# Kernel tuning notes

Hardware: AMD Instinct MI355X
Metric: run time of the kernel (lower is better)

Reference implementation:

```python
import jax, jax.numpy as jnp
import numpy as np

NUM_USERS = 100000
NUM_ITEMS = 50000
EMBED_DIM = 64
N_LAYERS = 3
SOCIAL_LAYERS = 2
NNZ_R = 3200000
NNZ_S = 2000000


def setup_inputs() -> dict:
    key = jax.random.key(0)
    ks = jax.random.split(key, 8)
    return {
        "user_emb": jax.random.normal(ks[0], (NUM_USERS, EMBED_DIM), jnp.float32) * 0.1,
        "item_emb": jax.random.normal(ks[1], (NUM_ITEMS, EMBED_DIM), jnp.float32) * 0.1,
        "r_vals": jax.random.uniform(ks[2], (NNZ_R,), jnp.float32) * 0.01,
        "s_vals": jax.random.uniform(ks[3], (NNZ_S,), jnp.float32) * 0.01,
        "r_rows": jax.random.randint(ks[4], (NNZ_R,), 0, NUM_USERS),
        "r_cols": jax.random.randint(ks[5], (NNZ_R,), 0, NUM_ITEMS),
        "s_rows": jax.random.randint(ks[6], (NNZ_S,), 0, NUM_USERS),
        "s_cols": jax.random.randint(ks[7], (NNZ_S,), 0, NUM_USERS),
    }


def spmm(rows, cols, vals, x, n_rows):
    # sparse(COO) @ dense: out[r] += v * x[c]
    return jax.ops.segment_sum(vals[:, None] * x[cols], rows, num_segments=n_rows)


def l2_normalize(x, eps=1e-12):
    return x / jnp.maximum(jnp.linalg.norm(x, axis=1, keepdims=True), eps)


def reference(user_emb, item_emb, r_vals, s_vals, r_rows, r_cols, s_rows, s_cols):
    # LightGCN-style propagation over user-item bipartite graph
    u, i = user_emb, item_emb
    u_sum, i_sum = user_emb, item_emb
    for _ in range(N_LAYERS):
        u_next = spmm(r_rows, r_cols, r_vals, i, NUM_USERS)   # R @ item
        i_next = spmm(r_cols, r_rows, r_vals, u, NUM_ITEMS)   # R^T @ user
        u, i = u_next, i_next  # dropout = identity in eval mode
        u_sum = u_sum + u
        i_sum = i_sum + i
    user_final = u_sum / (N_LAYERS + 1)
    item_final = i_sum / (N_LAYERS + 1)

    # social graph propagation on user embeddings
    s = user_emb
    s_sum = user_emb
    for _ in range(SOCIAL_LAYERS):
        s = spmm(s_rows, s_cols, s_vals, s, NUM_USERS)
        s_sum = s_sum + s
    social_final = s_sum / (SOCIAL_LAYERS + 1)

    final_user = l2_normalize(0.6 * user_final + 0.4 * social_final)
    final_item = l2_normalize(item_final)
    return final_user, final_item
```

## Files before the change

### kernel.cpp

```cpp
#include <hip/hip_runtime.h>

constexpr int NUM_USERS = 100000;
constexpr int NUM_ITEMS = 50000;
constexpr int DIM = 64;
constexpr int NNZ_R = 3200000;
constexpr int NNZ_S = 2000000;
constexpr int NNZ_TOT = NNZ_R + NNZ_R + NNZ_S;

constexpr int BSH_U = 8, BROWS_U = 256;
constexpr int BSH_I = 7, BROWS_I = 128;
constexpr int NC_U = (NUM_USERS + BROWS_U - 1) / BROWS_U;
constexpr int NC_I = (NUM_ITEMS + BROWS_I - 1) / BROWS_I;
constexpr int NC_S = NC_U;
constexpr int NC = NC_U + NC_I + NC_S;
constexpr int NBLK = 256;
constexpr int NPB = NBLK * NC;
constexpr int CHUNK_R = NNZ_R / NBLK;
constexpr int CHUNK_S = (NNZ_S + NBLK - 1) / NBLK;

constexpr int SB_EDGES = 4096;
constexpr int SB_PAIRS = 8192;

__device__ __forceinline__ float bf2f(unsigned short u) {
    return __uint_as_float((unsigned)u << 16);
}
__device__ __forceinline__ unsigned short f2bf(float f) {
    unsigned u = __float_as_uint(f);
    return (unsigned short)((u + 0x7FFFu + ((u >> 16) & 1u)) >> 16);
}
__device__ __forceinline__ float bflo(unsigned r) { return __uint_as_float(r << 16); }
__device__ __forceinline__ float bfhi(unsigned r) { return __uint_as_float(r & 0xFFFF0000u); }

__global__ __launch_bounds__(1024) void hist_lds(const int* __restrict__ rr,
                                                 const int* __restrict__ rc,
                                                 const int* __restrict__ sr,
                                                 int* __restrict__ cntPB ) {
    __shared__ int lds[NC];
    int k = blockIdx.x, tid = threadIdx.x;
    for (int c = tid; c < NC; c += 1024) lds[c] = 0;
    __syncthreads();
    int r0 = k * CHUNK_R, r1 = r0 + CHUNK_R;
    int s0 = k * CHUNK_S, s1 = min(s0 + CHUNK_S, NNZ_S);
    for (int i = r0 + tid; i < r1; i += 1024) {
        atomicAdd(&lds[rr[i] >> BSH_U], 1);
        atomicAdd(&lds[NC_U + (rc[i] >> BSH_I)], 1);
    }
    for (int i = s0 + tid; i < s1; i += 1024)
        atomicAdd(&lds[NC_U + NC_I + (sr[i] >> BSH_U)], 1);
    __syncthreads();
    for (int c = tid; c < NC; c += 1024) cntPB[c * NBLK + k] = lds[c];
}

__global__ __launch_bounds__(NBLK) void scan_bkt(int* __restrict__ cntPB,
                                                 int* __restrict__ bktTot) {
    int c = blockIdx.x, t = threadIdx.x;
    __shared__ int sh[NBLK];
    int v = cntPB[c * NBLK + t];
    sh[t] = v;
    __syncthreads();
    for (int off = 1; off < NBLK; off <<= 1) {
        int u = (t >= off) ? sh[t - off] : 0;
        __syncthreads();
        sh[t] += u;
        __syncthreads();
    }
    cntPB[c * NBLK + t] = sh[t] - v;
    if (t == NBLK - 1) bktTot[c] = sh[t];
}

__global__ __launch_bounds__(1024) void scan_top(int* __restrict__ B ) {
    __shared__ int part[1024];
    int t = threadIdx.x;
    const int chunk = (NC + 1023) >> 10;
    int lo = t * chunk, hi = min(lo + chunk, NC);
    int s = 0;
    for (int i = lo; i < hi; ++i) s += B[i];
    part[t] = s;
    __syncthreads();
    for (int off = 1; off < 1024; off <<= 1) {
        int v = (t >= off) ? part[t - off] : 0;
        __syncthreads();
        part[t] += v;
        __syncthreads();
    }
    int excl = (t == 0) ? 0 : part[t - 1];
    for (int i = lo; i < hi; ++i) {
        int v = B[i];
        B[i] = excl;
        excl += v;
    }
    if (t == 1023) B[NC] = part[1023];
}

__global__ __launch_bounds__(1024) void bin_pass(const int* __restrict__ rr,
                                                 const int* __restrict__ rc,
                                                 const float* __restrict__ rv,
                                                 const int* __restrict__ sr,
                                                 const int* __restrict__ sc,
                                                 const float* __restrict__ sv,
                                                 const int* __restrict__ cntPB,
                                                 const int* __restrict__ bktBase,
                                                 int2* __restrict__ ent) {
    __shared__ int cur[NC];
    __shared__ int cnt[NC];
    __shared__ int lstart[NC];
    __shared__ int lcur[NC];
    __shared__ int part[1024];
    __shared__ int2 stage[SB_PAIRS];
    __shared__ int gaddr[SB_PAIRS];
    int k = blockIdx.x, tid = threadIdx.x;
    for (int c = tid; c < NC; c += 1024)
        cur[c] = bktBase[c] + cntPB[c * NBLK + k];

    int r0 = k * CHUNK_R;
    for (int sb = 0; sb < CHUNK_R; sb += SB_EDGES) {
        int nE = min(SB_EDGES, CHUNK_R - sb);
        int base = r0 + sb;
        for (int c = tid; c < NC; c += 1024) { cnt[c] = 0; lcur[c] = 0; }
        __syncthreads();
        for (int i = tid; i < nE; i += 1024) {
            atomicAdd(&cnt[rr[base + i] >> BSH_U], 1);
            atomicAdd(&cnt[NC_U + (rc[base + i] >> BSH_I)], 1);
        }
        __syncthreads();
        int o0 = 2 * tid, o1 = 2 * tid + 1;
        int a = (o0 < NC) ? cnt[o0] : 0;
        int b = (o1 < NC) ? cnt[o1] : 0;
        part[tid] = a + b;
        __syncthreads();
        for (int off = 1; off < 1024; off <<= 1) {
            int v = (tid >= off) ? part[tid - off] : 0;
            __syncthreads();
            part[tid] += v;
            __syncthreads();
        }
        int ex = (tid == 0) ? 0 : part[tid - 1];
        if (o0 < NC) lstart[o0] = ex;
        if (o1 < NC) lstart[o1] = ex + a;
        __syncthreads();
        for (int i = tid; i < nE; i += 1024) {
            int r = rr[base + i], c = rc[base + i];
            int v = __float_as_int(rv[base + i]);
            int cu_ = r >> BSH_U;
            int j = atomicAdd(&lcur[cu_], 1);
            int lp = lstart[cu_] + j;
            stage[lp] = make_int2(((r & (BROWS_U - 1)) << 17) | c, v);
            gaddr[lp] = cur[cu_] + j;
            int ci_ = NC_U + (c >> BSH_I);
            int j2 = atomicAdd(&lcur[ci_], 1);
            int lp2 = lstart[ci_] + j2;
            stage[lp2] = make_int2(((c & (BROWS_I - 1)) << 17) | r, v);
            gaddr[lp2] = cur[ci_] + j2;
        }
        __syncthreads();
        int nP = 2 * nE;
        for (int s = tid; s < nP; s += 1024)
            ent[gaddr[s]] = stage[s];
        for (int c = tid; c < NC; c += 1024) cur[c] += cnt[c];
        __syncthreads();
    }

    int s0 = k * CHUNK_S, sEnd = min(s0 + CHUNK_S, NNZ_S);
    for (int sb = s0; sb < sEnd; sb += SB_PAIRS) {
        int nE = min(SB_PAIRS, sEnd - sb);
        for (int c = tid; c < NC; c += 1024) { cnt[c] = 0; lcur[c] = 0; }
        __syncthreads();
        for (int i = tid; i < nE; i += 1024)
            atomicAdd(&cnt[NC_U + NC_I + (sr[sb + i] >> BSH_U)], 1);
        __syncthreads();
        int o0 = 2 * tid, o1 = 2 * tid + 1;
        int a = (o0 < NC) ? cnt[o0] : 0;
        int b = (o1 < NC) ? cnt[o1] : 0;
        part[tid] = a + b;
        __syncthreads();
        for (int off = 1; off < 1024; off <<= 1) {
            int v = (tid >= off) ? part[tid - off] : 0;
            __syncthreads();
            part[tid] += v;
            __syncthreads();
        }
        int ex = (tid == 0) ? 0 : part[tid - 1];
        if (o0 < NC) lstart[o0] = ex;
        if (o1 < NC) lstart[o1] = ex + a;
        __syncthreads();
        for (int i = tid; i < nE; i += 1024) {
            int r = sr[sb + i];
            int cs_ = NC_U + NC_I + (r >> BSH_U);
            int j = atomicAdd(&lcur[cs_], 1);
            int lp = lstart[cs_] + j;
            stage[lp] = make_int2(((r & (BROWS_U - 1)) << 17) | sc[sb + i],
                                  __float_as_int(sv[sb + i]));
            gaddr[lp] = cur[cs_] + j;
        }
        __syncthreads();
        for (int s = tid; s < nE; s += 1024)
            ent[gaddr[s]] = stage[s];
        for (int c = tid; c < NC; c += 1024) cur[c] += cnt[c];
        __syncthreads();
    }
}

__global__ __launch_bounds__(512) void sort_buckets(const int2* __restrict__ src,
                                                    int2* __restrict__ dst,
                                                    const int* __restrict__ bktBase,
                                                    int* __restrict__ rPu,
                                                    int* __restrict__ rPi,
                                                    int* __restrict__ rPs) {
    int gb = blockIdx.x;
    int* rowptr;
    int brows, lb, nrows;
    if (gb < NC_U)              { rowptr = rPu; brows = BROWS_U; lb = gb;               nrows = NUM_USERS; }
    else if (gb < NC_U + NC_I)  { rowptr = rPi; brows = BROWS_I; lb = gb - NC_U;        nrows = NUM_ITEMS; }
    else                        { rowptr = rPs; brows = BROWS_U; lb = gb - NC_U - NC_I; nrows = NUM_USERS; }
    int t = threadIdx.x;
    __shared__ int cnt[256];
    __shared__ int part[256];
    __shared__ int ofs[256];
    if (t < 256) cnt[t] = 0;
    __syncthreads();
    int b0 = bktBase[gb], b1 = bktBase[gb + 1];
    for (int i = b0 + t; i < b1; i += 512)
        atomicAdd(&cnt[(unsigned)src[i].x >> 17], 1);
    __syncthreads();
    if (t < 256) part[t] = cnt[t];
    __syncthreads();
    for (int off = 1; off < 256; off <<= 1) {
        int v = 0;
        if (t < 256 && t >= off) v = part[t - off];
        __syncthreads();
        if (t < 256) part[t] += v;
        __syncthreads();
    }
    if (t < 256) ofs[t] = part[t] - cnt[t];
    __syncthreads();
    int gr = lb * brows + t;
    if (t < brows && gr < nrows) rowptr[gr] = b0 + ofs[t];
    if (gb == 0 && t == 0) {
        rPu[NUM_USERS] = NNZ_R;
        rPi[NUM_ITEMS] = 2 * NNZ_R;
        rPs[NUM_USERS] = NNZ_TOT;
    }
    __syncthreads();
    for (int i = b0 + t; i < b1; i += 512) {
        int2 v = src[i];
        int lr = (unsigned)v.x >> 17;
        int pos = b0 + atomicAdd(&ofs[lr], 1);
        dst[pos] = make_int2(v.x & 0x1FFFF, v.y);
    }
}

struct SpmmOp {
    const int* rowptr;
    const int2* ent;
    const unsigned short* x;
    unsigned short* out;
    float* acc;
    float w;
    int nrows;
};

__global__ __launch_bounds__(256, 4) void spmm2(SpmmOp A, SpmmOp B, int ablocks) {
    bool isA = (int)blockIdx.x < ablocks;
    SpmmOp op = isA ? A : B;
    int bid = isA ? blockIdx.x : blockIdx.x - ablocks;
    int row = bid * 4 + (threadIdx.x >> 6);
    if (row >= op.nrows) return;
    int lane = threadIdx.x & 63;
    int g = lane >> 4;
    int q = lane & 15;
    const int2* __restrict__ ent = op.ent;
    const unsigned short* __restrict__ x = op.x;
    int e = op.rowptr[row], end = op.rowptr[row + 1];
    float s0 = 0.f, s1 = 0.f, s2 = 0.f, s3 = 0.f;
    for (; e + 16 <= end; e += 16) {
        int2 n0 = ent[e + g];
        int2 n1 = ent[e + 4 + g];
        int2 n2 = ent[e + 8 + g];
        int2 n3 = ent[e + 12 + g];
        uint2 r0 = *reinterpret_cast<const uint2*>(x + (size_t)n0.x * DIM + q * 4);
        uint2 r1 = *reinterpret_cast<const uint2*>(x + (size_t)n1.x * DIM + q * 4);
        uint2 r2 = *reinterpret_cast<const uint2*>(x + (size_t)n2.x * DIM + q * 4);
        uint2 r3 = *reinterpret_cast<const uint2*>(x + (size_t)n3.x * DIM + q * 4);
        float v0 = __int_as_float(n0.y), v1 = __int_as_float(n1.y);
        float v2 = __int_as_float(n2.y), v3 = __int_as_float(n3.y);
        s0 += v0 * bflo(r0.x); s1 += v0 * bfhi(r0.x); s2 += v0 * bflo(r0.y); s3 += v0 * bfhi(r0.y);
        s0 += v1 * bflo(r1.x); s1 += v1 * bfhi(r1.x); s2 += v1 * bflo(r1.y); s3 += v1 * bfhi(r1.y);
        s0 += v2 * bflo(r2.x); s1 += v2 * bfhi(r2.x); s2 += v2 * bflo(r2.y); s3 += v2 * bfhi(r2.y);
        s0 += v3 * bflo(r3.x); s1 += v3 * bfhi(r3.x); s2 += v3 * bflo(r3.y); s3 += v3 * bfhi(r3.y);
    }
    if (e < end) {
        int t0 = e + 4 * g;
        int lim = end - 1;
        int c0 = min(t0, lim),     c1 = min(t0 + 1, lim);
        int c2 = min(t0 + 2, lim), c3 = min(t0 + 3, lim);
        int2 n0 = ent[c0];
        int2 n1 = ent[c1];
        int2 n2 = ent[c2];
        int2 n3 = ent[c3];
        uint2 r0 = *reinterpret_cast<const uint2*>(x + (size_t)n0.x * DIM + q * 4);
        uint2 r1 = *reinterpret_cast<const uint2*>(x + (size_t)n1.x * DIM + q * 4);
        uint2 r2 = *reinterpret_cast<const uint2*>(x + (size_t)n2.x * DIM + q * 4);
        uint2 r3 = *reinterpret_cast<const uint2*>(x + (size_t)n3.x * DIM + q * 4);
        float v0 = (t0     < end) ? __int_as_float(n0.y) : 0.f;
        float v1 = (t0 + 1 < end) ? __int_as_float(n1.y) : 0.f;
        float v2 = (t0 + 2 < end) ? __int_as_float(n2.y) : 0.f;
        float v3 = (t0 + 3 < end) ? __int_as_float(n3.y) : 0.f;
        s0 += v0 * bflo(r0.x); s1 += v0 * bfhi(r0.x); s2 += v0 * bflo(r0.y); s3 += v0 * bfhi(r0.y);
        s0 += v1 * bflo(r1.x); s1 += v1 * bfhi(r1.x); s2 += v1 * bflo(r1.y); s3 += v1 * bfhi(r1.y);
        s0 += v2 * bflo(r2.x); s1 += v2 * bfhi(r2.x); s2 += v2 * bflo(r2.y); s3 += v2 * bfhi(r2.y);
        s0 += v3 * bflo(r3.x); s1 += v3 * bfhi(r3.x); s2 += v3 * bflo(r3.y); s3 += v3 * bfhi(r3.y);
    }
    s0 += __shfl_xor(s0, 16, 64); s0 += __shfl_xor(s0, 32, 64);
    s1 += __shfl_xor(s1, 16, 64); s1 += __shfl_xor(s1, 32, 64);
    s2 += __shfl_xor(s2, 16, 64); s2 += __shfl_xor(s2, 32, 64);
    s3 += __shfl_xor(s3, 16, 64); s3 += __shfl_xor(s3, 32, 64);
    if (g == 0) {
        size_t base = (size_t)row * DIM + q * 4;
        if (op.out) {
            uint2 o;
            o.x = (unsigned)f2bf(s0) | ((unsigned)f2bf(s1) << 16);
            o.y = (unsigned)f2bf(s2) | ((unsigned)f2bf(s3) << 16);
            *reinterpret_cast<uint2*>(op.out + base) = o;
        }
        float4* a = reinterpret_cast<float4*>(op.acc + base);
        float4 av = *a;
        av.x += op.w * s0; av.y += op.w * s1; av.z += op.w * s2; av.w += op.w * s3;
        *a = av;
    }
}

__global__ void init_acc(const float* __restrict__ ue, const float* __restrict__ ie,
                         float* __restrict__ accU, float* __restrict__ accI,
                         unsigned short* __restrict__ ueB, unsigned short* __restrict__ ieB,
                         int u4, int i4) {
    const float wu = 0.6f / 4.0f + 0.4f / 3.0f;
    const float wi = 0.25f;
    int i = blockIdx.x * blockDim.x + threadIdx.x;
    int st = gridDim.x * blockDim.x;
    int n4 = u4 + i4;
    for (; i < n4; i += st) {
        if (i < u4) {
            float4 v = reinterpret_cast<const float4*>(ue)[i];
            reinterpret_cast<float4*>(accU)[i] = make_float4(wu * v.x, wu * v.y, wu * v.z, wu * v.w);
            ushort4 b;
            b.x = f2bf(v.x); b.y = f2bf(v.y); b.z = f2bf(v.z); b.w = f2bf(v.w);
            reinterpret_cast<ushort4*>(ueB)[i] = b;
        } else {
            int j = i - u4;
            float4 v = reinterpret_cast<const float4*>(ie)[j];
            reinterpret_cast<float4*>(accI)[j] = make_float4(wi * v.x, wi * v.y, wi * v.z, wi * v.w);
            ushort4 b;
            b.x = f2bf(v.x); b.y = f2bf(v.y); b.z = f2bf(v.z); b.w = f2bf(v.w);
            reinterpret_cast<ushort4*>(ieB)[j] = b;
        }
    }
}

__global__ void finalize_kernel(float* __restrict__ out, int nrows) {
    int row = blockIdx.x * 4 + (threadIdx.x >> 6);
    if (row >= nrows) return;
    int d = threadIdx.x & 63;
    int idx = row * DIM + d;
    float val = out[idx];
    float sq = val * val;
    #pragma unroll
    for (int off = 32; off; off >>= 1) sq += __shfl_xor(sq, off, 64);
    out[idx] = val / fmaxf(sqrtf(sq), 1e-12f);
}

extern "C" void kernel_launch(void* const* d_in, const int* in_sizes, int n_in,
                              void* d_out, int out_size, void* d_ws, size_t ws_size,
                              hipStream_t stream) {
    const float* user_emb = (const float*)d_in[0];
    const float* item_emb = (const float*)d_in[1];
    const float* r_vals   = (const float*)d_in[2];
    const float* s_vals   = (const float*)d_in[3];
    const int*   r_rows   = (const int*)d_in[4];
    const int*   r_cols   = (const int*)d_in[5];
    const int*   s_rows   = (const int*)d_in[6];
    const int*   s_cols   = (const int*)d_in[7];

    const size_t U = (size_t)NUM_USERS * DIM;
    const size_t I = (size_t)NUM_ITEMS * DIM;

    int2* ent_sorted = (int2*)d_ws;
    char* region2 = (char*)(ent_sorted + NNZ_TOT);
    int2* ent_bin = (int2*)region2;
    unsigned short* ueB = (unsigned short*)region2;
    unsigned short* ieB = ueB + U;
    unsigned short* uA  = ieB + I;
    unsigned short* uB  = uA + U;
    unsigned short* iA  = uB + U;
    unsigned short* iB  = iA + I;
    int* cntPB   = (int*)(region2 + (size_t)NNZ_TOT * 8);
    int* bktBase = cntPB + NPB;
    int* rPu = bktBase + NC + 1;
    int* rPi = rPu + NUM_USERS + 1;
    int* rPs = rPi + NUM_ITEMS + 1;

    float* accU = (float*)d_out;
    float* accI = (float*)d_out + U;

    dim3 blk(256);

    hist_lds<<<NBLK, 1024, 0, stream>>>(r_rows, r_cols, s_rows, cntPB);
    scan_bkt<<<NC, NBLK, 0, stream>>>(cntPB, bktBase);
    scan_top<<<1, 1024, 0, stream>>>(bktBase);
    bin_pass<<<NBLK, 1024, 0, stream>>>(r_rows, r_cols, r_vals, s_rows, s_cols, s_vals,
                                        cntPB, bktBase, ent_bin);
    sort_buckets<<<NC, 512, 0, stream>>>(ent_bin, ent_sorted, bktBase, rPu, rPi, rPs);

    init_acc<<<2048, blk, 0, stream>>>(user_emb, item_emb, accU, accI, ueB, ieB,
                                       (int)(U / 4), (int)(I / 4));

    const float WU = 0.6f / 4.0f, WI = 0.25f, WS = 0.4f / 3.0f;
    int ub = (NUM_USERS + 3) / 4, ib = (NUM_ITEMS + 3) / 4;

    SpmmOp u1{rPu, ent_sorted, ieB, uA, accU, WU, NUM_USERS};
    SpmmOp i1{rPi, ent_sorted, ueB, iA, accI, WI, NUM_ITEMS};
    spmm2<<<ub + ib, blk, 0, stream>>>(u1, i1, ub);

    SpmmOp u2{rPu, ent_sorted, iA, uB, accU, WU, NUM_USERS};
    SpmmOp i2{rPi, ent_sorted, uA, iB, accI, WI, NUM_ITEMS};
    spmm2<<<ub + ib, blk, 0, stream>>>(u2, i2, ub);

    SpmmOp u3{rPu, ent_sorted, iB, nullptr, accU, WU, NUM_USERS};
    SpmmOp i3{rPi, ent_sorted, uB, nullptr, accI, WI, NUM_ITEMS};
    spmm2<<<ub + ib, blk, 0, stream>>>(u3, i3, ub);

    SpmmOp so1{rPs, ent_sorted, ueB, uA, accU, WS, NUM_USERS};
    spmm2<<<ub, blk, 0, stream>>>(so1, so1, ub);
    SpmmOp so2{rPs, ent_sorted, uA, nullptr, accU, WS, NUM_USERS};
    spmm2<<<ub, blk, 0, stream>>>(so2, so2, ub);

    finalize_kernel<<<(NUM_USERS + NUM_ITEMS + 3) / 4, blk, 0, stream>>>(
        (float*)d_out, NUM_USERS + NUM_ITEMS);
}
```

Before: 643.4 us.

## Fold accumulator init and final-layer accumulation into SpMM and finalize kernels

The fp32 accumulator initialisation moves out of the standalone init kernel and into the first SpMM layer, which now reads the bf16 input embeddings. The last item/user layer and the second social layer now write bf16 outputs instead of doing a read-modify-write on the fp32 accumulator, and the finalize kernel adds those bf16 results before normalising. This cuts fp32 accumulator traffic and reorders the launches so the social layers run before the third layer. The trade-off is a new bf16 scratch buffer, reuse of the existing ones, and slightly lower precision from adding bf16-rounded layer outputs.

```diff
diff --git a/kernel.cpp b/kernel.cpp
--- a/kernel.cpp
+++ b/kernel.cpp
@@ -255,7 +255,9 @@
     const unsigned short* x;
     unsigned short* out;
     float* acc;
+    const unsigned short* initsrc;
     float w;
+    float w0;
     int nrows;
 };
 
@@ -322,33 +324,37 @@
             o.y = (unsigned)f2bf(s2) | ((unsigned)f2bf(s3) << 16);
             *reinterpret_cast<uint2*>(op.out + base) = o;
         }
-        float4* a = reinterpret_cast<float4*>(op.acc + base);
-        float4 av = *a;
-        av.x += op.w * s0; av.y += op.w * s1; av.z += op.w * s2; av.w += op.w * s3;
-        *a = av;
-    }
-}
-
-__global__ void init_acc(const float* __restrict__ ue, const float* __restrict__ ie,
-                         float* __restrict__ accU, float* __restrict__ accI,
-                         unsigned short* __restrict__ ueB, unsigned short* __restrict__ ieB,
-                         int u4, int i4) {
-    const float wu = 0.6f / 4.0f + 0.4f / 3.0f;
-    const float wi = 0.25f;
+        if (op.acc) {
+            float4* a = reinterpret_cast<float4*>(op.acc + base);
+            float4 av;
+            if (op.initsrc) {
+                uint2 iv = *reinterpret_cast<const uint2*>(op.initsrc + base);
+                av.x = op.w0 * bflo(iv.x); av.y = op.w0 * bfhi(iv.x);
+                av.z = op.w0 * bflo(iv.y); av.w = op.w0 * bfhi(iv.y);
+            } else {
+                av = *a;
+            }
+            av.x += op.w * s0; av.y += op.w * s1; av.z += op.w * s2; av.w += op.w * s3;
+            *a = av;
+        }
+    }
+}
+
+__global__ void to_bf16(const float* __restrict__ ue, const float* __restrict__ ie,
+                        unsigned short* __restrict__ ueB, unsigned short* __restrict__ ieB,
+                        int u4, int i4) {
     int i = blockIdx.x * blockDim.x + threadIdx.x;
     int st = gridDim.x * blockDim.x;
     int n4 = u4 + i4;
     for (; i < n4; i += st) {
         if (i < u4) {
             float4 v = reinterpret_cast<const float4*>(ue)[i];
-            reinterpret_cast<float4*>(accU)[i] = make_float4(wu * v.x, wu * v.y, wu * v.z, wu * v.w);
             ushort4 b;
             b.x = f2bf(v.x); b.y = f2bf(v.y); b.z = f2bf(v.z); b.w = f2bf(v.w);
             reinterpret_cast<ushort4*>(ueB)[i] = b;
         } else {
             int j = i - u4;
             float4 v = reinterpret_cast<const float4*>(ie)[j];
-            reinterpret_cast<float4*>(accI)[j] = make_float4(wi * v.x, wi * v.y, wi * v.z, wi * v.w);
             ushort4 b;
             b.x = f2bf(v.x); b.y = f2bf(v.y); b.z = f2bf(v.z); b.w = f2bf(v.w);
             reinterpret_cast<ushort4*>(ieB)[j] = b;
@@ -356,12 +362,22 @@
     }
 }
 
-__global__ void finalize_kernel(float* __restrict__ out, int nrows) {
+__global__ void finalize_kernel(float* __restrict__ out,
+                                const unsigned short* __restrict__ uC,
+                                const unsigned short* __restrict__ s2,
+                                const unsigned short* __restrict__ iC) {
+    const float WU = 0.6f / 4.0f, WS = 0.4f / 3.0f, WI = 0.25f;
     int row = blockIdx.x * 4 + (threadIdx.x >> 6);
-    if (row >= nrows) return;
+    if (row >= NUM_USERS + NUM_ITEMS) return;
     int d = threadIdx.x & 63;
-    int idx = row * DIM + d;
+    size_t idx = (size_t)row * DIM + d;
     float val = out[idx];
+    if (row < NUM_USERS) {
+        val += WU * bf2f(uC[idx]) + WS * bf2f(s2[idx]);
+    } else {
+        size_t iidx = idx - (size_t)NUM_USERS * DIM;
+        val += WI * bf2f(iC[iidx]);
+    }
     float sq = val * val;
     #pragma unroll
     for (int off = 32; off; off >>= 1) sq += __shfl_xor(sq, off, 64);
@@ -392,7 +408,11 @@
     unsigned short* uB  = uA + U;
     unsigned short* iA  = uB + U;
     unsigned short* iB  = iA + I;
-    int* cntPB   = (int*)(region2 + (size_t)NNZ_TOT * 8);
+    unsigned short* uC  = iB + I;
+    unsigned short* s1b = uA;
+    unsigned short* s2b = ueB;
+    unsigned short* iCb = ieB;
+    int* cntPB   = (int*)(uC + U);
     int* bktBase = cntPB + NPB;
     int* rPu = bktBase + NC + 1;
     int* rPi = rPu + NUM_USERS + 1;
@@ -410,29 +430,31 @@
                                         cntPB, bktBase, ent_bin);
     sort_buckets<<<NC, 512, 0, stream>>>(ent_bin, ent_sorted, bktBase, rPu, rPi, rPs);
 
-    init_acc<<<2048, blk, 0, stream>>>(user_emb, item_emb, accU, accI, ueB, ieB,
-                                       (int)(U / 4), (int)(I / 4));
+    to_bf16<<<2048, blk, 0, stream>>>(user_emb, item_emb, ueB, ieB,
+                                      (int)(U / 4), (int)(I / 4));
 
     const float WU = 0.6f / 4.0f, WI = 0.25f, WS = 0.4f / 3.0f;
+    const float WU0 = WU + WS;
     int ub = (NUM_USERS + 3) / 4, ib = (NUM_ITEMS + 3) / 4;
 
-    SpmmOp u1{rPu, ent_sorted, ieB, uA, accU, WU, NUM_USERS};
-    SpmmOp i1{rPi, ent_sorted, ueB, iA, accI, WI, NUM_ITEMS};
+    SpmmOp u1{rPu, ent_sorted, ieB, uA, accU, ueB, WU, WU0, NUM_USERS};
+    SpmmOp i1{rPi, ent_sorted, ueB, iA, accI, ieB, WI, WI, NUM_ITEMS};
     spmm2<<<ub + ib, blk, 0, stream>>>(u1, i1, ub);
 
-    SpmmOp u2{rPu, ent_sorted, iA, uB, accU, WU, NUM_USERS};
-    SpmmOp i2{rPi, ent_sorted, uA, iB, accI, WI, NUM_ITEMS};
+    SpmmOp u2{rPu, ent_sorted, iA, uB, accU, nullptr, WU, 0.f, NUM_USERS};
+    SpmmOp i2{rPi, ent_sorted, uA, iB, accI, nullptr, WI, 0.f, NUM_ITEMS};
     spmm2<<<ub + ib, blk, 0, stream>>>(u2, i2, ub);
 
-    SpmmOp u3{rPu, ent_sorted, iB, nullptr, accU, WU, NUM_USERS};
-    SpmmOp i3{rPi, ent_sorted, uB, nullptr, accI, WI, NUM_ITEMS};
+    SpmmOp so1{rPs, ent_sorted, ueB, s1b, accU, nullptr, WS, 0.f, NUM_USERS};
+    spmm2<<<ub, blk, 0, stream>>>(so1, so1, ub);
+
+    SpmmOp so2{rPs, ent_sorted, s1b, s2b, nullptr, nullptr, 0.f, 0.f, NUM_USERS};
+    spmm2<<<ub, blk, 0, stream>>>(so2, so2, ub);
+
+    SpmmOp u3{rPu, ent_sorted, iB, uC, nullptr, nullptr, 0.f, 0.f, NUM_USERS};
+    SpmmOp i3{rPi, ent_sorted, uB, iCb, nullptr, nullptr, 0.f, 0.f, NUM_ITEMS};
     spmm2<<<ub + ib, blk, 0, stream>>>(u3, i3, ub);
 
-    SpmmOp so1{rPs, ent_sorted, ueB, uA, accU, WS, NUM_USERS};
-    spmm2<<<ub, blk, 0, stream>>>(so1, so1, ub);
-    SpmmOp so2{rPs, ent_sorted, uA, nullptr, accU, WS, NUM_USERS};
-    spmm2<<<ub, blk, 0, stream>>>(so2, so2, ub);
-
     finalize_kernel<<<(NUM_USERS + NUM_ITEMS + 3) / 4, blk, 0, stream>>>(
-        (float*)d_out, NUM_USERS + NUM_ITEMS);
-}
+        (float*)d_out, uC, s2b, iCb);
+}
```

New measurement: 633.0 us, median of 2. About the same (-1.6%).
